# Optimization experiments

Hardware: AMD Instinct MI355X
Metric: run time of the kernel (lower is better)

Reference implementation:

```python
import jax, jax.numpy as jnp
import numpy as np

INPUT_SIZE = 2048
HIDDEN_SIZE = 2048
BATCH = 4096


def setup_inputs() -> dict:
    key = jax.random.key(0)
    ks = jax.random.split(key, 12)
    std = 1.0 / HIDDEN_SIZE ** 0.5
    def u(k, shape):
        return jax.random.uniform(k, shape, jnp.float32, -std, std)
    inp = {
        "x": jax.random.normal(ks[0], (BATCH, INPUT_SIZE), jnp.float32),
        "h": jax.random.normal(ks[1], (BATCH, HIDDEN_SIZE), jnp.float32),
        "c": jax.random.normal(ks[2], (BATCH, HIDDEN_SIZE), jnp.float32),
        "weight_ii": u(ks[3], (HIDDEN_SIZE, INPUT_SIZE)),
        "weight_if": u(ks[4], (HIDDEN_SIZE, INPUT_SIZE)),
        "weight_ig": u(ks[5], (HIDDEN_SIZE, INPUT_SIZE)),
        "weight_io": u(ks[6], (HIDDEN_SIZE, INPUT_SIZE)),
        "weight_hi": u(ks[7], (HIDDEN_SIZE, HIDDEN_SIZE)),
        "weight_hf": u(ks[8], (HIDDEN_SIZE, HIDDEN_SIZE)),
        "weight_hg": u(ks[9], (HIDDEN_SIZE, HIDDEN_SIZE)),
        "weight_ho": u(ks[10], (HIDDEN_SIZE, HIDDEN_SIZE)),
        "bias_i": u(ks[11], (HIDDEN_SIZE,)),
        "bias_f": u(jax.random.fold_in(key, 100), (HIDDEN_SIZE,)),
        "bias_g": u(jax.random.fold_in(key, 101), (HIDDEN_SIZE,)),
        "bias_o": u(jax.random.fold_in(key, 102), (HIDDEN_SIZE,)),
    }
    return inp


def reference(x, h, c, weight_ii, weight_if, weight_ig, weight_io,
              weight_hi, weight_hf, weight_hg, weight_ho,
              bias_i, bias_f, bias_g, bias_o):
    # Fuse the 4 input projections and 4 hidden projections into 2 GEMMs
    # (same math as 8 separate matmuls in the original module).
    W_x = jnp.concatenate([weight_ii, weight_if, weight_ig, weight_io], axis=0)  # [4H, I]
    W_h = jnp.concatenate([weight_hi, weight_hf, weight_hg, weight_ho], axis=0)  # [4H, H]
    b = jnp.concatenate([bias_i, bias_f, bias_g, bias_o], axis=0)                # [4H]
    gates = x @ W_x.T + h @ W_h.T + b                                            # [B, 4H]
    gi, gf, gg, go = jnp.split(gates, 4, axis=1)
    i = jax.nn.sigmoid(gi)
    f = jax.nn.sigmoid(gf)
    g = jnp.tanh(gg)
    o = jax.nn.sigmoid(go)
    c_new = f * c + i * g
    h_new = o * jnp.tanh(c_new)
    return (h_new, c_new)
```

## Files before the change

kernel.cpp:

```cpp
#include <hip/hip_runtime.h>
#include <cstdint>
#include <cstddef>

#define BATCH 4096
#define HID   2048

typedef __attribute__((ext_vector_type(8))) short bf16x8;
typedef __attribute__((ext_vector_type(4))) float f32x4;

__device__ __forceinline__ unsigned short f2bf(float f) {
  union { float f; unsigned u; } a; a.f = f;
  unsigned u = a.u;
  return (unsigned short)((u + 0x7FFFu + ((u >> 16) & 1u)) >> 16);
}

__device__ __forceinline__ void gload_lds16(const void* g, void* l) {
  __builtin_amdgcn_global_load_lds((const __attribute__((address_space(1))) void*)g,
                                   (__attribute__((address_space(3))) void*)l, 16, 0, 0);
}

#define SCHED0() __builtin_amdgcn_sched_barrier(0)
#define SBAR()  do { SCHED0(); __builtin_amdgcn_s_barrier(); SCHED0(); } while (0)
#define WAITV(N) do { SCHED0(); asm volatile("s_waitcnt vmcnt(" #N ")" ::: "memory"); SCHED0(); } while (0)
#define WAITL(N) do { SCHED0(); asm volatile("s_waitcnt lgkmcnt(" #N ")" ::: "memory"); SCHED0(); } while (0)
#define DSR(dst, adr, IMM) asm volatile("ds_read_b128 %0, %1 offset:" #IMM : "=v"(dst) : "v"(adr))

#define RD16(AS, BS) do { \
  unsigned aA_ = aBase + (unsigned)o_n, bB_ = bBase + (unsigned)o_n; \
  DSR(AS[0],aA_,0);    DSR(AS[1],aA_,1024); DSR(AS[2],aA_,2048); DSR(AS[3],aA_,3072); \
  DSR(AS[4],aA_,4096); DSR(AS[5],aA_,5120); DSR(AS[6],aA_,6144); DSR(AS[7],aA_,7168); \
  DSR(BS[0],bB_,0);    DSR(BS[1],bB_,1024); DSR(BS[2],bB_,2048); DSR(BS[3],bB_,3072); \
  DSR(BS[4],bB_,4096); DSR(BS[5],bB_,5120); DSR(BS[6],bB_,6144); DSR(BS[7],bB_,7168); \
} while (0)

#define MFMA64(AS, BS) do { _Pragma("unroll") \
  for (int m_ = 0; m_ < 8; m_++) { _Pragma("unroll") \
    for (int n_ = 0; n_ < 8; n_++) \
      acc[m_][n_] = __builtin_amdgcn_mfma_f32_16x16x32_bf16(AS[m_], BS[n_], acc[m_][n_], 0, 0, 0); } \
} while (0)

#define STAGE_G(KOFF, DOF) do { \
  gload_lds16(pA + (KOFF),          dA + (DOF)); \
  gload_lds16(pA + 262144 + (KOFF), dA + (DOF) + 4096); \
  gload_lds16(pA + 524288 + (KOFF), dA + (DOF) + 8192); \
  gload_lds16(pA + 786432 + (KOFF), dA + (DOF) + 12288); \
  gload_lds16(pB + (KOFF),          dA + (DOF) + 16384); \
  gload_lds16(pB + 65536 + (KOFF),  dA + (DOF) + 20480); \
  gload_lds16(pB + 131072 + (KOFF), dA + (DOF) + 24576); \
  gload_lds16(pB + 196608 + (KOFF), dA + (DOF) + 28672); \
} while (0)

#define ADVR(o) do { (o) = ((o) + 32768) & 131071; } while (0)

#define SLOT(VW, STG, ACUR, BCUR, ANXT, BNXT) do { \
  VW; \
  SBAR(); \
  WAITL(0); \
  RD16(ANXT, BNXT); \
  STG; \
  SCHED0(); \
  __builtin_amdgcn_s_setprio(1); MFMA64(ACUR, BCUR); __builtin_amdgcn_s_setprio(0); \
  ADVR(o_c); ADVR(o_n); ADVR(o_s); koff += 32; \
} while (0)

__global__ __launch_bounds__(256) void convert_kernel(
    const float* __restrict__ x, const float* __restrict__ h,
    const float* __restrict__ wii, const float* __restrict__ wif,
    const float* __restrict__ wig, const float* __restrict__ wio,
    const float* __restrict__ whi, const float* __restrict__ whf,
    const float* __restrict__ whg, const float* __restrict__ who,
    unsigned short* __restrict__ Abf, unsigned short* __restrict__ Wbf) {
  int seg = blockIdx.y;
  const float* src;
  unsigned short* dst;
  int ofs;
  size_t rofs;
  if (seg < 4) {
    src = (seg < 2) ? x : h;
    dst = Abf;
    ofs = (seg < 2) ? 0 : 2048;
    rofs = (seg & 1) ? 2048 : 0;
    src += rofs * 2048;
  } else {
    int g = (seg - 4) & 3;
    dst = Wbf + (size_t)g * 2048 * 4096;
    ofs = (seg >= 8) ? 2048 : 0;
    rofs = 0;
    switch (seg) {
      case 4: src = wii; break; case 5: src = wif; break;
      case 6: src = wig; break; case 7: src = wio; break;
      case 8: src = whi; break; case 9: src = whf; break;
      case 10: src = whg; break; default: src = who; break;
    }
  }
  size_t idx = (size_t)blockIdx.x * 256 + threadIdx.x;
  size_t e = idx * 4;
  int n = (int)(e >> 11);
  int k = (int)(e & 2047);
  float4 v = *(const float4*)(src + e);
  ushort4 o;
  o.x = f2bf(v.x); o.y = f2bf(v.y); o.z = f2bf(v.z); o.w = f2bf(v.w);
  *(ushort4*)(dst + (rofs + (size_t)n) * 4096 + ofs + k) = o;
}

__global__ __launch_bounds__(256, 1) void lstm_gemm4(
    const unsigned short* __restrict__ Abf, const unsigned short* __restrict__ Wbf,
    const float* __restrict__ c_in,
    const float* __restrict__ bias_i, const float* __restrict__ bias_f,
    const float* __restrict__ bias_g, const float* __restrict__ bias_o,
    float* __restrict__ out) {
  __shared__ unsigned short lds[4 * 16384];

  int tid = threadIdx.x;
  int lane = tid & 63;
  int wid = tid >> 6;
  int wr = wid >> 1;
  int wc = wid & 1;
  int lrow = lane & 15;
  int qh = lane >> 4;

  int bid = blockIdx.x;
  int xcd = bid & 7;
  int t7 = bid >> 3;
  int mt = t7 & 15;
  int bn = xcd * 4 + (t7 >> 4);
  int m0 = mt * 256;

  int r0 = tid >> 2, cc0 = tid & 3;
  int ccs0 = cc0 ^ ((r0 >> 1) & 3);
  const unsigned short* pA = Abf + (size_t)(m0 + r0) * 4096 + ccs0 * 8;
  int g0 = (r0 >> 4) & 3;
  const unsigned short* pB = Wbf + ((size_t)g0 * 2048 + bn * 64 + (r0 & 15)) * 4096 + ccs0 * 8;

  char* L0 = (char*)&lds[0];
  char* dA = L0 + tid * 16;
  unsigned ldsOff = (unsigned)(size_t)(__attribute__((address_space(3))) char*)L0;

  unsigned qs = ((unsigned)(qh ^ ((lrow >> 1) & 3))) << 4;
  unsigned aBase = ldsOff + (unsigned)(wr * 128 + lrow) * 64 + qs;
  unsigned bBase = ldsOff + 16384u + (unsigned)(wc * 128 + lrow) * 64 + qs;

  f32x4 acc[8][8];
  #pragma unroll
  for (int a = 0; a < 8; a++)
    #pragma unroll
    for (int b = 0; b < 8; b++) acc[a][b] = (f32x4){0.f, 0.f, 0.f, 0.f};

  bf16x8 aA[8], bA[8], aB[8], bB[8];

  int o_c = 0, o_n = 32768, o_s = 98304;
  int koff = 96;

  STAGE_G(0, 0);
  STAGE_G(32, 32768);
  STAGE_G(64, 65536);
  WAITV(16);
  SBAR();
  { int sv = o_n; o_n = 0; RD16(aA, bA); o_n = sv; }

  for (int i = 0; i < 62; ++i) {
    SLOT(WAITV(8), STAGE_G(koff, o_s), aA, bA, aB, bB);
    SLOT(WAITV(8), STAGE_G(koff, o_s), aB, bB, aA, bA);
  }
  SLOT(WAITV(8), STAGE_G(koff, o_s), aA, bA, aB, bB);
  SLOT(WAITV(8), (void)0, aB, bB, aA, bA);
  SLOT(WAITV(0), (void)0, aA, bA, aB, bB);
  WAITL(0);
  __builtin_amdgcn_s_setprio(1); MFMA64(aB, bB); __builtin_amdgcn_s_setprio(0);

  int jb = bn * 64 + wc * 32 + lrow;
  int rbase = m0 + wr * 128 + qh * 4;
  #pragma unroll
  for (int jj2 = 0; jj2 < 2; jj2++) {
    int j = jb + jj2 * 16;
    float bi = bias_i[j], bff = bias_f[j], bgg = bias_g[j], bo = bias_o[j];
    #pragma unroll
    for (int mf = 0; mf < 8; mf++) {
      #pragma unroll
      for (int qq = 0; qq < 4; qq++) {
        int m = rbase + mf * 16 + qq;
        size_t off = (size_t)m * HID + j;
        float gi = acc[mf][jj2 * 4 + 0][qq] + bi;
        float gf = acc[mf][jj2 * 4 + 1][qq] + bff;
        float gg = acc[mf][jj2 * 4 + 2][qq] + bgg;
        float go = acc[mf][jj2 * 4 + 3][qq] + bo;
        float iv = 1.f / (1.f + __expf(-gi));
        float fv = 1.f / (1.f + __expf(-gf));
        float gv = tanhf(gg);
        float ov = 1.f / (1.f + __expf(-go));
        float cn = fv * c_in[off] + iv * gv;
        float hn = ov * tanhf(cn);
        out[off] = hn;
        out[(size_t)BATCH * HID + off] = cn;
      }
    }
  }
}

__global__ __launch_bounds__(256) void lstm_gemm_fb(
    const float* __restrict__ x, const float* __restrict__ h,
    const float* __restrict__ wii, const float* __restrict__ wif,
    const float* __restrict__ wig, const float* __restrict__ wio,
    const float* __restrict__ whi, const float* __restrict__ whf,
    const float* __restrict__ whg, const float* __restrict__ who,
    const float* __restrict__ c_in,
    const float* __restrict__ bias_i, const float* __restrict__ bias_f,
    const float* __restrict__ bias_g, const float* __restrict__ bias_o,
    float* __restrict__ out) {
  __shared__ unsigned short Ald[128 * 64];
  __shared__ unsigned short Bld[128 * 64];
  int tid = threadIdx.x;
  int lane = tid & 63;
  int wid = tid >> 6;
  int wr = wid >> 1, wc = wid & 1;
  int bid = blockIdx.x;
  int swz = (bid & 7) * 256 + (bid >> 3);
  int mt = swz & 31;
  int ht = swz >> 5;
  int m0 = mt * 128;
  int j0 = ht * 32;
  f32x4 acc[4][4];
  #pragma unroll
  for (int a = 0; a < 4; a++)
    #pragma unroll
    for (int b = 0; b < 4; b++) acc[a][b] = (f32x4){0.f, 0.f, 0.f, 0.f};
  int lrow = lane & 15;
  int lsw = lrow & 7;
  int qbase = lane >> 4;
  for (int kt = 0; kt < 64; kt++) {
    int k0 = kt * 64;
    const float* Asrc = (k0 < 2048) ? x : h;
    int ka = k0 & 2047;
    #pragma unroll
    for (int i = 0; i < 4; i++) {
      int c = i * 256 + tid;
      int r = c >> 3, cc = c & 7;
      int ccs = cc ^ (r & 7);
      const float* s = Asrc + (size_t)(m0 + r) * 2048 + ka + ccs * 8;
      float4 v0 = *(const float4*)s;
      float4 v1 = *(const float4*)(s + 4);
      bf16x8 pk;
      pk[0] = (short)f2bf(v0.x); pk[1] = (short)f2bf(v0.y);
      pk[2] = (short)f2bf(v0.z); pk[3] = (short)f2bf(v0.w);
      pk[4] = (short)f2bf(v1.x); pk[5] = (short)f2bf(v1.y);
      pk[6] = (short)f2bf(v1.z); pk[7] = (short)f2bf(v1.w);
      *(bf16x8*)((char*)Ald + (size_t)c * 16) = pk;
    }
    #pragma unroll
    for (int i = 0; i < 4; i++) {
      int c = i * 256 + tid;
      int rb = c >> 3, cc = c & 7;
      int ccs = cc ^ (rb & 7);
      int g = rb >> 5, jj = rb & 31;
      const float* Bsrc;
      if (k0 < 2048) Bsrc = (g == 0) ? wii : (g == 1) ? wif : (g == 2) ? wig : wio;
      else           Bsrc = (g == 0) ? whi : (g == 1) ? whf : (g == 2) ? whg : who;
      const float* s = Bsrc + (size_t)(j0 + jj) * 2048 + ka + ccs * 8;
      float4 v0 = *(const float4*)s;
      float4 v1 = *(const float4*)(s + 4);
      bf16x8 pk;
      pk[0] = (short)f2bf(v0.x); pk[1] = (short)f2bf(v0.y);
      pk[2] = (short)f2bf(v0.z); pk[3] = (short)f2bf(v0.w);
      pk[4] = (short)f2bf(v1.x); pk[5] = (short)f2bf(v1.y);
      pk[6] = (short)f2bf(v1.z); pk[7] = (short)f2bf(v1.w);
      *(bf16x8*)((char*)Bld + (size_t)c * 16) = pk;
    }
    __syncthreads();
    #pragma unroll
    for (int ks = 0; ks < 2; ks++) {
      int q = ks * 4 + qbase;
      int qs8 = (q ^ lsw) * 8;
      bf16x8 af[4], bg[4];
      #pragma unroll
      for (int mf = 0; mf < 4; mf++)
        af[mf] = *(const bf16x8*)&Ald[(wr * 64 + mf * 16 + lrow) * 64 + qs8];
      #pragma unroll
      for (int g = 0; g < 4; g++)
        bg[g] = *(const bf16x8*)&Bld[(g * 32 + wc * 16 + lrow) * 64 + qs8];
      #pragma unroll
      for (int mf = 0; mf < 4; mf++)
        #pragma unroll
        for (int g = 0; g < 4; g++)
          acc[mf][g] = __builtin_amdgcn_mfma_f32_16x16x32_bf16(af[mf], bg[g], acc[mf][g], 0, 0, 0);
    }
    __syncthreads();
  }
  int j = j0 + wc * 16 + lrow;
  float bi = bias_i[j], bff = bias_f[j], bgg = bias_g[j], bo = bias_o[j];
  int rbase = m0 + wr * 64 + (lane >> 4) * 4;
  #pragma unroll
  for (int mf = 0; mf < 4; mf++) {
    #pragma unroll
    for (int q = 0; q < 4; q++) {
      int m = rbase + mf * 16 + q;
      size_t off = (size_t)m * HID + j;
      float gi = acc[mf][0][q] + bi;
      float gf = acc[mf][1][q] + bff;
      float gg = acc[mf][2][q] + bgg;
      float go = acc[mf][3][q] + bo;
      float iv = 1.f / (1.f + __expf(-gi));
      float fv = 1.f / (1.f + __expf(-gf));
      float gv = tanhf(gg);
      float ov = 1.f / (1.f + __expf(-go));
      float cn = fv * c_in[off] + iv * gv;
      float hn = ov * tanhf(cn);
      out[off] = hn;
      out[(size_t)BATCH * HID + off] = cn;
    }
  }
}

extern "C" void kernel_launch(void* const* d_in, const int* in_sizes, int n_in,
                              void* d_out, int out_size, void* d_ws, size_t ws_size,
                              hipStream_t stream) {
  const float* x   = (const float*)d_in[0];
  const float* h   = (const float*)d_in[1];
  const float* c   = (const float*)d_in[2];
  const float* wii = (const float*)d_in[3];
  const float* wif = (const float*)d_in[4];
  const float* wig = (const float*)d_in[5];
  const float* wio = (const float*)d_in[6];
  const float* whi = (const float*)d_in[7];
  const float* whf = (const float*)d_in[8];
  const float* whg = (const float*)d_in[9];
  const float* who = (const float*)d_in[10];
  const float* bi  = (const float*)d_in[11];
  const float* bf  = (const float*)d_in[12];
  const float* bg  = (const float*)d_in[13];
  const float* bo  = (const float*)d_in[14];
  float* out = (float*)d_out;

  size_t needA = (size_t)4096 * 4096 * 2;
  size_t needW = (size_t)8192 * 4096 * 2;

  if (ws_size >= needA + needW) {
    unsigned short* Abf = (unsigned short*)d_ws;
    unsigned short* Wbf = (unsigned short*)((char*)d_ws + needA);
    convert_kernel<<<dim3(4096, 12), 256, 0, stream>>>(
        x, h, wii, wif, wig, wio, whi, whf, whg, who, Abf, Wbf);
    lstm_gemm4<<<512, 256, 0, stream>>>(Abf, Wbf, c, bi, bf, bg, bo, out);
  } else {
    lstm_gemm_fb<<<2048, 256, 0, stream>>>(
        x, h, wii, wif, wig, wio, whi, whf, whg, who,
        c, bi, bf, bg, bo, out);
  }
}
```

Before: 354.7 us.

## Switch GEMM to 32x32x16 MFMA with 8-wave blocks

Replaces the 16x16x32 MFMA tiling with 32x32x16 bf16 MFMAs. The block grows to 512 threads (8 waves), and each wave computes a 64x128 tile instead of 128x128. Per-thread staging loads drop from 8 to 4 and LDS reads from 16 to 12 per k-step, with launch bounds asking for two blocks per CU. The aim is fewer LDS reads per FLOP and more waves to hide latency. The risks are register pressure under the new bounds, whether two blocks fit given the shared-memory size, and the changed LDS swizzle access pattern.

```diff
diff --git a/kernel.cpp b/kernel.cpp
--- a/kernel.cpp
+++ b/kernel.cpp
@@ -7,6 +7,7 @@
 
 typedef __attribute__((ext_vector_type(8))) short bf16x8;
 typedef __attribute__((ext_vector_type(4))) float f32x4;
+typedef __attribute__((ext_vector_type(16))) float f32x16;
 
 __device__ __forceinline__ unsigned short f2bf(float f) {
   union { float f; unsigned u; } a; a.f = f;
@@ -24,31 +25,29 @@
 #define WAITV(N) do { SCHED0(); asm volatile("s_waitcnt vmcnt(" #N ")" ::: "memory"); SCHED0(); } while (0)
 #define WAITL(N) do { SCHED0(); asm volatile("s_waitcnt lgkmcnt(" #N ")" ::: "memory"); SCHED0(); } while (0)
 #define DSR(dst, adr, IMM) asm volatile("ds_read_b128 %0, %1 offset:" #IMM : "=v"(dst) : "v"(adr))
-
-#define RD16(AS, BS) do { \
-  unsigned aA_ = aBase + (unsigned)o_n, bB_ = bBase + (unsigned)o_n; \
-  DSR(AS[0],aA_,0);    DSR(AS[1],aA_,1024); DSR(AS[2],aA_,2048); DSR(AS[3],aA_,3072); \
-  DSR(AS[4],aA_,4096); DSR(AS[5],aA_,5120); DSR(AS[6],aA_,6144); DSR(AS[7],aA_,7168); \
-  DSR(BS[0],bB_,0);    DSR(BS[1],bB_,1024); DSR(BS[2],bB_,2048); DSR(BS[3],bB_,3072); \
-  DSR(BS[4],bB_,4096); DSR(BS[5],bB_,5120); DSR(BS[6],bB_,6144); DSR(BS[7],bB_,7168); \
+#define PRIO1() __builtin_amdgcn_s_setprio(1)
+#define PRIO0() __builtin_amdgcn_s_setprio(0)
+
+#define RD12(AS, BS) do { \
+  unsigned a0_ = adrA + (unsigned)o_n, a1_ = a0_ ^ 32u; \
+  unsigned b0_ = adrB + (unsigned)o_n, b1_ = b0_ ^ 32u; \
+  DSR(AS[0],a0_,0);    DSR(AS[1],a1_,0);    DSR(AS[2],a0_,2048); DSR(AS[3],a1_,2048); \
+  DSR(BS[0],b0_,0);    DSR(BS[1],b1_,0);    DSR(BS[2],b0_,2048); DSR(BS[3],b1_,2048); \
+  DSR(BS[4],b0_,4096); DSR(BS[5],b1_,4096); DSR(BS[6],b0_,6144); DSR(BS[7],b1_,6144); \
 } while (0)
 
-#define MFMA64(AS, BS) do { _Pragma("unroll") \
-  for (int m_ = 0; m_ < 8; m_++) { _Pragma("unroll") \
-    for (int n_ = 0; n_ < 8; n_++) \
-      acc[m_][n_] = __builtin_amdgcn_mfma_f32_16x16x32_bf16(AS[m_], BS[n_], acc[m_][n_], 0, 0, 0); } \
-} while (0)
+#define MFMA16(AS, BS) do { _Pragma("unroll") \
+  for (int mf_ = 0; mf_ < 2; mf_++) { _Pragma("unroll") \
+    for (int g_ = 0; g_ < 4; g_++) { \
+      acc[mf_][g_] = __builtin_amdgcn_mfma_f32_32x32x16_bf16(AS[2*mf_],   BS[2*g_],   acc[mf_][g_], 0, 0, 0); \
+      acc[mf_][g_] = __builtin_amdgcn_mfma_f32_32x32x16_bf16(AS[2*mf_+1], BS[2*g_+1], acc[mf_][g_], 0, 0, 0); \
+    } } } while (0)
 
 #define STAGE_G(KOFF, DOF) do { \
-  gload_lds16(pA + (KOFF),          dA + (DOF)); \
-  gload_lds16(pA + 262144 + (KOFF), dA + (DOF) + 4096); \
-  gload_lds16(pA + 524288 + (KOFF), dA + (DOF) + 8192); \
-  gload_lds16(pA + 786432 + (KOFF), dA + (DOF) + 12288); \
-  gload_lds16(pB + (KOFF),          dA + (DOF) + 16384); \
-  gload_lds16(pB + 65536 + (KOFF),  dA + (DOF) + 20480); \
-  gload_lds16(pB + 131072 + (KOFF), dA + (DOF) + 24576); \
-  gload_lds16(pB + 196608 + (KOFF), dA + (DOF) + 28672); \
-} while (0)
+  gload_lds16(pA + (KOFF),          dD + (DOF)); \
+  gload_lds16(pA + 524288 + (KOFF), dD + (DOF) + 8192); \
+  gload_lds16(pB + (KOFF),          dD + (DOF) + 16384); \
+  gload_lds16(pB + 131072 + (KOFF), dD + (DOF) + 24576); } while (0)
 
 #define ADVR(o) do { (o) = ((o) + 32768) & 131071; } while (0)
 
@@ -56,11 +55,11 @@
   VW; \
   SBAR(); \
   WAITL(0); \
-  RD16(ANXT, BNXT); \
+  RD12(ANXT, BNXT); \
   STG; \
   SCHED0(); \
-  __builtin_amdgcn_s_setprio(1); MFMA64(ACUR, BCUR); __builtin_amdgcn_s_setprio(0); \
-  ADVR(o_c); ADVR(o_n); ADVR(o_s); koff += 32; \
+  PRIO1(); MFMA16(ACUR, BCUR); PRIO0(); \
+  ADVR(o_n); ADVR(o_s); koff += 32; \
 } while (0)
 
 __global__ __launch_bounds__(256) void convert_kernel(
@@ -103,7 +102,7 @@
   *(ushort4*)(dst + (rofs + (size_t)n) * 4096 + ofs + k) = o;
 }
 
-__global__ __launch_bounds__(256, 1) void lstm_gemm4(
+__global__ __launch_bounds__(512, 2) void lstm_gemm32(
     const unsigned short* __restrict__ Abf, const unsigned short* __restrict__ Wbf,
     const float* __restrict__ c_in,
     const float* __restrict__ bias_i, const float* __restrict__ bias_f,
@@ -116,8 +115,8 @@
   int wid = tid >> 6;
   int wr = wid >> 1;
   int wc = wid & 1;
-  int lrow = lane & 15;
-  int qh = lane >> 4;
+  int l31 = lane & 31;
+  int hi = lane >> 5;
 
   int bid = blockIdx.x;
   int xcd = bid & 7;
@@ -129,70 +128,70 @@
   int r0 = tid >> 2, cc0 = tid & 3;
   int ccs0 = cc0 ^ ((r0 >> 1) & 3);
   const unsigned short* pA = Abf + (size_t)(m0 + r0) * 4096 + ccs0 * 8;
-  int g0 = (r0 >> 4) & 3;
-  const unsigned short* pB = Wbf + ((size_t)g0 * 2048 + bn * 64 + (r0 & 15)) * 4096 + ccs0 * 8;
+  const unsigned short* pB = Wbf + ((size_t)(r0 >> 5) * 2048 + bn * 64 + (r0 & 31)) * 4096 + ccs0 * 8;
 
   char* L0 = (char*)&lds[0];
-  char* dA = L0 + tid * 16;
+  char* dD = L0 + tid * 16;
   unsigned ldsOff = (unsigned)(size_t)(__attribute__((address_space(3))) char*)L0;
 
-  unsigned qs = ((unsigned)(qh ^ ((lrow >> 1) & 3))) << 4;
-  unsigned aBase = ldsOff + (unsigned)(wr * 128 + lrow) * 64 + qs;
-  unsigned bBase = ldsOff + 16384u + (unsigned)(wc * 128 + lrow) * 64 + qs;
-
-  f32x4 acc[8][8];
+  unsigned key = ((unsigned)l31 >> 1) & 3u;
+  unsigned ch0 = ((unsigned)hi ^ key) << 4;
+  unsigned adrA = ldsOff + (unsigned)(wr * 64 + l31) * 64 + ch0;
+  unsigned adrB = ldsOff + 16384u + (unsigned)(wc * 128 + l31) * 64 + ch0;
+
+  f32x16 acc[2][4];
   #pragma unroll
-  for (int a = 0; a < 8; a++)
-    #pragma unroll
-    for (int b = 0; b < 8; b++) acc[a][b] = (f32x4){0.f, 0.f, 0.f, 0.f};
-
-  bf16x8 aA[8], bA[8], aB[8], bB[8];
-
-  int o_c = 0, o_n = 32768, o_s = 98304;
+  for (int a = 0; a < 2; a++)
+    #pragma unroll
+    for (int b = 0; b < 4; b++)
+      #pragma unroll
+      for (int e = 0; e < 16; e++) acc[a][b][e] = 0.f;
+
+  bf16x8 aA[4], bA[8], aB[4], bB[8];
+
+  int o_n = 32768;
+  int o_s = 98304;
   int koff = 96;
 
   STAGE_G(0, 0);
   STAGE_G(32, 32768);
   STAGE_G(64, 65536);
-  WAITV(16);
+  WAITV(8);
   SBAR();
-  { int sv = o_n; o_n = 0; RD16(aA, bA); o_n = sv; }
+  { int sv = o_n; o_n = 0; RD12(aA, bA); o_n = sv; }
 
   for (int i = 0; i < 62; ++i) {
-    SLOT(WAITV(8), STAGE_G(koff, o_s), aA, bA, aB, bB);
-    SLOT(WAITV(8), STAGE_G(koff, o_s), aB, bB, aA, bA);
-  }
-  SLOT(WAITV(8), STAGE_G(koff, o_s), aA, bA, aB, bB);
-  SLOT(WAITV(8), (void)0, aB, bB, aA, bA);
+    SLOT(WAITV(4), STAGE_G(koff, o_s), aA, bA, aB, bB);
+    SLOT(WAITV(4), STAGE_G(koff, o_s), aB, bB, aA, bA);
+  }
+  SLOT(WAITV(4), STAGE_G(koff, o_s), aA, bA, aB, bB);
+  SLOT(WAITV(4), (void)0, aB, bB, aA, bA);
   SLOT(WAITV(0), (void)0, aA, bA, aB, bB);
   WAITL(0);
-  __builtin_amdgcn_s_setprio(1); MFMA64(aB, bB); __builtin_amdgcn_s_setprio(0);
-
-  int jb = bn * 64 + wc * 32 + lrow;
-  int rbase = m0 + wr * 128 + qh * 4;
+  SCHED0();
+  PRIO1(); MFMA16(aB, bB); PRIO0();
+
+  int j = bn * 64 + wc * 32 + l31;
+  float bi = bias_i[j], bff = bias_f[j], bgg = bias_g[j], bo = bias_o[j];
+  int rb0 = m0 + wr * 64 + hi * 4;
   #pragma unroll
-  for (int jj2 = 0; jj2 < 2; jj2++) {
-    int j = jb + jj2 * 16;
-    float bi = bias_i[j], bff = bias_f[j], bgg = bias_g[j], bo = bias_o[j];
-    #pragma unroll
-    for (int mf = 0; mf < 8; mf++) {
-      #pragma unroll
-      for (int qq = 0; qq < 4; qq++) {
-        int m = rbase + mf * 16 + qq;
-        size_t off = (size_t)m * HID + j;
-        float gi = acc[mf][jj2 * 4 + 0][qq] + bi;
-        float gf = acc[mf][jj2 * 4 + 1][qq] + bff;
-        float gg = acc[mf][jj2 * 4 + 2][qq] + bgg;
-        float go = acc[mf][jj2 * 4 + 3][qq] + bo;
-        float iv = 1.f / (1.f + __expf(-gi));
-        float fv = 1.f / (1.f + __expf(-gf));
-        float gv = tanhf(gg);
-        float ov = 1.f / (1.f + __expf(-go));
-        float cn = fv * c_in[off] + iv * gv;
-        float hn = ov * tanhf(cn);
-        out[off] = hn;
-        out[(size_t)BATCH * HID + off] = cn;
-      }
+  for (int mf = 0; mf < 2; mf++) {
+    #pragma unroll
+    for (int reg = 0; reg < 16; reg++) {
+      int m = rb0 + mf * 32 + (reg & 3) + 8 * (reg >> 2);
+      size_t off = (size_t)m * HID + j;
+      float gi = acc[mf][0][reg] + bi;
+      float gf = acc[mf][1][reg] + bff;
+      float gg = acc[mf][2][reg] + bgg;
+      float go = acc[mf][3][reg] + bo;
+      float iv = 1.f / (1.f + __expf(-gi));
+      float fv = 1.f / (1.f + __expf(-gf));
+      float gv = tanhf(gg);
+      float ov = 1.f / (1.f + __expf(-go));
+      float cn = fv * c_in[off] + iv * gv;
+      float hn = ov * tanhf(cn);
+      out[off] = hn;
+      out[(size_t)BATCH * HID + off] = cn;
     }
   }
 }
@@ -338,7 +337,7 @@
     unsigned short* Wbf = (unsigned short*)((char*)d_ws + needA);
     convert_kernel<<<dim3(4096, 12), 256, 0, stream>>>(
         x, h, wii, wif, wig, wio, whi, whf, whg, who, Abf, Wbf);
-    lstm_gemm4<<<512, 256, 0, stream>>>(Abf, Wbf, c, bi, bf, bg, bo, out);
+    lstm_gemm32<<<512, 512, 0, stream>>>(Abf, Wbf, c, bi, bf, bg, bo, out);
   } else {
     lstm_gemm_fb<<<2048, 256, 0, stream>>>(
         x, h, wii, wif, wig, wio, whi, whf, whg, who,
```

Result: no change. 349.1 us (-1.6%).
